# Performance work log

Measured on AMD Instinct MI355X. Metric: run time of the kernel, lower is better.

## Reference

```python
import jax, jax.numpy as jnp
import numpy as np

B, N, M, LDIM, RDIM, AGG = 4, 512, 512, 512, 512, 256


def setup_inputs() -> dict:
    key = jax.random.key(0)
    ks = jax.random.split(key, 7)
    data = jax.random.normal(ks[0], (B, N, LDIM), dtype=jnp.float32)
    crit = jax.random.normal(ks[1], (B, M, RDIM), dtype=jnp.float32)
    Wl = jax.random.normal(ks[2], (LDIM, AGG), dtype=jnp.float32) / np.sqrt(LDIM)
    bl = jax.random.normal(ks[3], (AGG,), dtype=jnp.float32) * 0.01
    Wr = jax.random.normal(ks[4], (RDIM, AGG), dtype=jnp.float32) / np.sqrt(RDIM)
    br = jax.random.normal(ks[5], (AGG,), dtype=jnp.float32) * 0.01
    agg = jax.random.uniform(ks[6], (AGG,), dtype=jnp.float32, minval=-0.01, maxval=0.01)
    return {"data": data, "crit": crit, "Wl": Wl, "bl": bl, "Wr": Wr, "br": br, "agg": agg}


def reference(data, crit, Wl, bl, Wr, br, agg):
    # linear projections
    datalin = jnp.einsum('bnl,la->bna', data, Wl) + bl   # [B,N,A]
    critlin = jnp.einsum('bmr,ra->bma', crit, Wr) + br   # [B,M,A]
    # broadcast add -> tanh -> reduce with agg vector: [B,N,M]
    linsum = jnp.tanh(datalin[:, :, None, :] + critlin[:, None, :, :])  # [B,N,M,A]
    dists = jnp.einsum('bnma,a->bnm', linsum, agg)
    return dists
```

## Files before the change

kernel.cpp:

```cpp
#include <hip/hip_runtime.h>


#define A_DIM 256
#define K_DIM 512
#define NROWS 2048

typedef unsigned short ushort;
typedef __attribute__((ext_vector_type(4))) unsigned short us4;
typedef __attribute__((ext_vector_type(8))) unsigned short us8;
typedef __attribute__((ext_vector_type(8))) short short8;
typedef __attribute__((ext_vector_type(4))) float f32x4;
typedef __attribute__((ext_vector_type(2))) float f32x2;

__device__ inline ushort f2bf(float x) {
    union { float f; unsigned u; } v; v.f = x;
    unsigned r = v.u + 0x7FFFu + ((v.u >> 16) & 1u);
    return (ushort)(r >> 16);
}
__device__ inline float bf2f(ushort h) {
    union { unsigned u; float f; } v; v.u = ((unsigned)h) << 16; return v.f;
}
__device__ inline unsigned pack2bf(float lo, float hi) {
    return (unsigned)f2bf(lo) | ((unsigned)f2bf(hi) << 16);
}
__device__ inline f32x2 fma2(f32x2 a, f32x2 b, f32x2 c) {
    return __builtin_elementwise_fma(a, b, c);
}

__global__ __launch_bounds__(256) void transpose_w_kernel(
    const float* __restrict__ Wl, const float* __restrict__ Wr,
    ushort* __restrict__ wt)
{
    __shared__ float tile[64][68];
    const int t   = threadIdx.x;
    const int bid = blockIdx.x;
    const int at  = bid & 3;
    const int kt  = (bid >> 2) & 7;
    const int src = bid >> 5;
    const int a0 = at * 64, k0 = kt * 64;
    const float* W = src ? Wr : Wl;
    ushort* out = wt + (size_t)src * (A_DIM * K_DIM);

    const int c4 = (t & 15) * 4;
    const int kr = t >> 4;
#pragma unroll
    for (int r = 0; r < 4; r++) {
        const int k = kr + r * 16;
        *(float4*)&tile[k][c4] = *(const float4*)(W + (size_t)(k0 + k) * A_DIM + a0 + c4);
    }
    __syncthreads();
    const int aL  = t & 63;
    const int ks0 = (t >> 6) * 16;
#pragma unroll
    for (int g = 0; g < 4; g++) {
        us4 o;
#pragma unroll
        for (int i = 0; i < 4; i++) o[i] = f2bf(tile[ks0 + g * 4 + i][aL]);
        __builtin_nontemporal_store(o, (us4*)(out + (size_t)(a0 + aL) * K_DIM + k0 + ks0 + g * 4));
    }
}

__global__ __launch_bounds__(256) void proj_mfma_kernel(
    const float* __restrict__ data, const float* __restrict__ crit,
    const float* __restrict__ bl, const float* __restrict__ br,
    const ushort* __restrict__ wt, ushort* __restrict__ eplanes)
{
    __shared__ ushort Ws[64][520];

    const int t   = threadIdx.x;
    const int bid = blockIdx.x;
    const int ct  = bid >> 7;
    const int rt  = bid & 127;
    const int src = rt >> 6;
    const int lr0 = (rt & 63) * 32;
    const int c0  = ct * 64;

    const float* X    = src ? crit : data;
    const float* bias = src ? br : bl;
    const ushort* Wt  = wt + (size_t)src * (A_DIM * K_DIM);
    ushort* E = eplanes + (size_t)src * ((size_t)A_DIM * NROWS);

    const int lane = t & 63;
    const int wid  = t >> 6;
    const int wm   = wid >> 1, wn = wid & 1;
    const int quad = lane >> 4, l16 = lane & 15;

    const float* xrow = X + (size_t)(lr0 + wm * 16 + l16) * K_DIM + quad * 8;
    const int aloc0 = wn * 32 + l16;

    f32x4 acc0 = {0.f, 0.f, 0.f, 0.f}, acc1 = {0.f, 0.f, 0.f, 0.f};

    {
        const int a  = t & 63;
        const int ks = (t >> 6) * 128;
        const ushort* s = Wt + (size_t)(c0 + a) * K_DIM + ks;
#pragma unroll
        for (int i = 0; i < 16; i++)
            *(us8*)&Ws[a][ks + i * 8] = *(const us8*)(s + i * 8);
    }

    float4 pa0 = *(const float4*)(xrow);
    float4 pb0 = *(const float4*)(xrow + 4);
    float4 pa1 = *(const float4*)(xrow + 32);
    float4 pb1 = *(const float4*)(xrow + 36);

    __syncthreads();

#pragma unroll
    for (int s = 0; s < 16; s++) {
        float4 ca = pa0, cb = pb0;
        pa0 = pa1; pb0 = pb1;
        if (s < 14) {
            pa1 = *(const float4*)(xrow + (s + 2) * 32);
            pb1 = *(const float4*)(xrow + (s + 2) * 32 + 4);
        }
        union { short8 s8; unsigned u[4]; } af;
        af.u[0] = pack2bf(ca.x, ca.y);
        af.u[1] = pack2bf(ca.z, ca.w);
        af.u[2] = pack2bf(cb.x, cb.y);
        af.u[3] = pack2bf(cb.z, cb.w);
        short8 b0 = *(const short8*)&Ws[aloc0     ][s * 32 + quad * 8];
        short8 b1 = *(const short8*)&Ws[aloc0 + 16][s * 32 + quad * 8];
        acc0 = __builtin_amdgcn_mfma_f32_16x16x32_bf16(af.s8, b0, acc0, 0, 0, 0);
        acc1 = __builtin_amdgcn_mfma_f32_16x16x32_bf16(af.s8, b1, acc1, 0, 0, 0);
    }

    const float c2 = 2.8853900817779268f;
    const int a_col0 = c0 + wn * 32 + l16;
    const int a_col1 = a_col0 + 16;
    const int row0   = lr0 + wm * 16 + quad * 4;
    const float bv0 = bias[a_col0], bv1 = bias[a_col1];
    us4 e0, e1;
#pragma unroll
    for (int i = 0; i < 4; i++) {
        float v0 = (acc0[i] + bv0) * c2;
        float v1 = (acc1[i] + bv1) * c2;
        v0 = fminf(fmaxf(v0, -15.f), 15.f);
        v1 = fminf(fmaxf(v1, -15.f), 15.f);
        e0[i] = f2bf(__builtin_amdgcn_exp2f(v0));
        e1[i] = f2bf(__builtin_amdgcn_exp2f(v1));
    }
    __builtin_nontemporal_store(e0, (us4*)(E + (size_t)a_col0 * NROWS + row0));
    __builtin_nontemporal_store(e1, (us4*)(E + (size_t)a_col1 * NROWS + row0));
}

__global__ __launch_bounds__(1024) void tanh_reduce_kernel(
    const ushort* __restrict__ eplanes, const float* __restrict__ agg,
    float* __restrict__ out)
{
    __shared__ __align__(16) float et [4][64][68];
    __shared__ __align__(16) float ect[4][64][68];
    __shared__ __align__(16) float aggs[256];

    const int t  = threadIdx.x;
    const int h  = t >> 8;
    const int u  = t & 255;
    const int m0 = blockIdx.x * 64;
    const int n0 = blockIdx.y * 64;
    const int b  = blockIdx.z;

    const size_t PLANE = (size_t)A_DIM * NROWS;
    const ushort* Ed = eplanes;
    const ushort* Ec = eplanes + PLANE;
    const int row_n = b * 512 + n0;
    const int row_m = b * 512 + m0;

    const int tx = u & 15;
    const int ty = u >> 4;

    if (t < 256) aggs[t] = 2.0f * agg[t];

    f32x2 acc2[4][2];
#pragma unroll
    for (int i = 0; i < 4; i++) { acc2[i][0] = (f32x2)0.f; acc2[i][1] = (f32x2)0.f; }
    float sagg = 0.f;

    const int aL = u >> 2;
    const int qd = u & 3;

    float (*eth)[68]  = et[h];
    float (*ecth)[68] = ect[h];

    {
        const size_t base = (size_t)(h * 64 + aL) * NROWS;
        us4 pn[4], pm[4];
#pragma unroll
        for (int r = 0; r < 4; r++) {
            pn[r] = *(const us4*)(Ed + base + row_n + qd * 16 + r * 4);
            pm[r] = *(const us4*)(Ec + base + row_m + qd * 16 + r * 4);
        }
#pragma unroll
        for (int r = 0; r < 4; r++) {
            float4 ev, cv;
            ev.x = bf2f(pn[r][0]); ev.y = bf2f(pn[r][1]);
            ev.z = bf2f(pn[r][2]); ev.w = bf2f(pn[r][3]);
            cv.x = bf2f(pm[r][0]); cv.y = bf2f(pm[r][1]);
            cv.z = bf2f(pm[r][2]); cv.w = bf2f(pm[r][3]);
            *(float4*)&eth [aL][qd * 16 + r * 4] = ev;
            *(float4*)&ecth[aL][qd * 16 + r * 4] = cv;
        }
    }
    __syncthreads();

    for (int qg = 0; qg < 16; qg++) {
        const float4 ag = *(const float4*)&aggs[h * 64 + qg * 4];
        sagg += (ag.x + ag.y) + (ag.z + ag.w);
        float  en[4][4];
        f32x2  fm[4][2];
#pragma unroll
        for (int v = 0; v < 4; v++) {
            float4 e4 = *(const float4*)&eth [qg * 4 + v][ty * 4];
            float4 f4 = *(const float4*)&ecth[qg * 4 + v][tx * 4];
            en[v][0] = e4.x; en[v][1] = e4.y; en[v][2] = e4.z; en[v][3] = e4.w;
            fm[v][0] = f32x2{f4.x, f4.y};
            fm[v][1] = f32x2{f4.z, f4.w};
        }
#pragma unroll
        for (int i = 0; i < 4; i++)
#pragma unroll
            for (int jp = 0; jp < 2; jp++) {
                const f32x2 one = (f32x2)1.f;
                f32x2 q0 = fma2((f32x2)en[0][i], fm[0][jp], one);
                f32x2 q1 = fma2((f32x2)en[1][i], fm[1][jp], one);
                f32x2 q2 = fma2((f32x2)en[2][i], fm[2][jp], one);
                f32x2 q3 = fma2((f32x2)en[3][i], fm[3][jp], one);
                f32x2 q01 = q0 * q1, q23 = q2 * q3;
                f32x2 n01 = fma2((f32x2)ag.x, q1, (f32x2)ag.y * q0);
                f32x2 n23 = fma2((f32x2)ag.z, q3, (f32x2)ag.w * q2);
                f32x2 N   = fma2(n01, q23, n23 * q01);
                f32x2 D   = q01 * q23;
                f32x2 r;
                r.x = __builtin_amdgcn_rcpf(D.x);
                r.y = __builtin_amdgcn_rcpf(D.y);
                acc2[i][jp] = fma2(N, r, acc2[i][jp]);
            }
    }

    const float base = 0.5f * sagg;
    float* xb = (float*)ect;
    __syncthreads();
    if (h != 0) {
        float* w = xb + ((size_t)(h - 1) * 256 + u) * 17;
#pragma unroll
        for (int i = 0; i < 4; i++)
#pragma unroll
            for (int jp = 0; jp < 2; jp++) {
                w[i * 4 + jp * 2 + 0] = base - acc2[i][jp].x;
                w[i * 4 + jp * 2 + 1] = base - acc2[i][jp].y;
            }
    }
    __syncthreads();
    if (h == 0) {
        const float* x1 = xb + (size_t)u * 17;
        const float* x2 = xb + ((size_t)256 + u) * 17;
        const float* x3 = xb + ((size_t)512 + u) * 17;
#pragma unroll
        for (int i = 0; i < 4; i++) {
            f32x4 v;
            v.x = ((base - acc2[i][0].x) + x1[i * 4 + 0]) + (x2[i * 4 + 0] + x3[i * 4 + 0]);
            v.y = ((base - acc2[i][0].y) + x1[i * 4 + 1]) + (x2[i * 4 + 1] + x3[i * 4 + 1]);
            v.z = ((base - acc2[i][1].x) + x1[i * 4 + 2]) + (x2[i * 4 + 2] + x3[i * 4 + 2]);
            v.w = ((base - acc2[i][1].y) + x1[i * 4 + 3]) + (x2[i * 4 + 3] + x3[i * 4 + 3]);
            __builtin_nontemporal_store(v,
                (f32x4*)(out + ((size_t)(b * 512 + n0 + ty * 4 + i) * 512) + m0 + tx * 4));
        }
    }
}

extern "C" void kernel_launch(void* const* d_in, const int* in_sizes, int n_in,
                              void* d_out, int out_size, void* d_ws, size_t ws_size,
                              hipStream_t stream) {
    const float* data = (const float*)d_in[0];
    const float* crit = (const float*)d_in[1];
    const float* Wl   = (const float*)d_in[2];
    const float* bl   = (const float*)d_in[3];
    const float* Wr   = (const float*)d_in[4];
    const float* br   = (const float*)d_in[5];
    const float* agg  = (const float*)d_in[6];
    float* out = (float*)d_out;

    ushort* eplanes = (ushort*)d_ws;
    ushort* wt      = eplanes + 2 * (size_t)A_DIM * NROWS;

    transpose_w_kernel<<<dim3(64), 256, 0, stream>>>(Wl, Wr, wt);

    proj_mfma_kernel<<<dim3(512), 256, 0, stream>>>(data, crit, bl, br, wt, eplanes);

    tanh_reduce_kernel<<<dim3(8, 8, 4), 1024, 0, stream>>>(eplanes, agg, out);
}
```

Before: 107.2 us.

## Fuse transpose, projection and tanh-reduce into one cooperative kernel

Merges the three kernels into a single cooperative launch of 256 blocks of 1024 threads, with grid.sync between the weight transpose, the MFMA projection and the tanh-reduce phases. Each phase is re-tiled so it fits 256 blocks: the transpose uses 16-wide tiles and the projection uses 64-row tiles with one MFMA accumulator per wave. Shared memory is shared between phases through a union. This removes two kernel launch gaps, at the cost of grid-wide barriers and smaller per-block work in the early phases.

```diff
diff --git a/kernel.cpp b/kernel.cpp
--- a/kernel.cpp
+++ b/kernel.cpp
@@ -1,4 +1,7 @@
 #include <hip/hip_runtime.h>
+#include <hip/hip_cooperative_groups.h>
+
+namespace cg = cooperative_groups;
 
 
 #define A_DIM 256
@@ -27,242 +30,223 @@
     return __builtin_elementwise_fma(a, b, c);
 }
 
-__global__ __launch_bounds__(256) void transpose_w_kernel(
-    const float* __restrict__ Wl, const float* __restrict__ Wr,
-    ushort* __restrict__ wt)
+__global__ __launch_bounds__(1024) void fused_fd_kernel(
+    const float* __restrict__ data, const float* __restrict__ crit,
+    const float* __restrict__ Wl, const float* __restrict__ bl,
+    const float* __restrict__ Wr, const float* __restrict__ br,
+    const float* __restrict__ agg,
+    ushort* __restrict__ wt, ushort* __restrict__ eplanes,
+    float* __restrict__ out)
 {
-    __shared__ float tile[64][68];
+    __shared__ __align__(16) union {
+        float tile[64][17];
+        ushort Ws[64][520];
+        struct { float et[4][64][68]; float ect[4][64][68];
+                 float aggs[256]; } p2;
+    } sm;
+
     const int t   = threadIdx.x;
     const int bid = blockIdx.x;
-    const int at  = bid & 3;
-    const int kt  = (bid >> 2) & 7;
-    const int src = bid >> 5;
-    const int a0 = at * 64, k0 = kt * 64;
-    const float* W = src ? Wr : Wl;
-    ushort* out = wt + (size_t)src * (A_DIM * K_DIM);
-
-    const int c4 = (t & 15) * 4;
-    const int kr = t >> 4;
-#pragma unroll
-    for (int r = 0; r < 4; r++) {
-        const int k = kr + r * 16;
-        *(float4*)&tile[k][c4] = *(const float4*)(W + (size_t)(k0 + k) * A_DIM + a0 + c4);
+    cg::grid_group grid = cg::this_grid();
+
+    {
+        const int at  = bid & 15;
+        const int kt  = (bid >> 4) & 7;
+        const int src = bid >> 7;
+        const int a0 = at * 16, k0 = kt * 64;
+        const float* W = src ? Wr : Wl;
+        ushort* o = wt + (size_t)src * (A_DIM * K_DIM);
+
+        const int k = t >> 4, ai = t & 15;
+        sm.tile[k][ai] = W[(size_t)(k0 + k) * A_DIM + a0 + ai];
+        __syncthreads();
+        const int a2 = t >> 6, kk = t & 63;
+        __builtin_nontemporal_store(f2bf(sm.tile[kk][a2]),
+                                    o + (size_t)(a0 + a2) * K_DIM + k0 + kk);
     }
-    __syncthreads();
-    const int aL  = t & 63;
-    const int ks0 = (t >> 6) * 16;
-#pragma unroll
-    for (int g = 0; g < 4; g++) {
-        us4 o;
-#pragma unroll
-        for (int i = 0; i < 4; i++) o[i] = f2bf(tile[ks0 + g * 4 + i][aL]);
-        __builtin_nontemporal_store(o, (us4*)(out + (size_t)(a0 + aL) * K_DIM + k0 + ks0 + g * 4));
+    grid.sync();
+
+    {
+        const int rt  = bid & 63;
+        const int ct  = bid >> 6;
+        const int src = rt >> 5;
+        const int lr0 = (rt & 31) * 64;
+        const int c0  = ct * 64;
+
+        const float* X    = src ? crit : data;
+        const float* bias = src ? br : bl;
+        const ushort* Wt  = wt + (size_t)src * (A_DIM * K_DIM);
+        ushort* E = eplanes + (size_t)src * ((size_t)A_DIM * NROWS);
+
+        const int lane = t & 63;
+        const int wid  = t >> 6;
+        const int wm   = wid >> 2, wn = wid & 3;
+        const int quad = lane >> 4, l16 = lane & 15;
+
+        const float* xrow = X + (size_t)(lr0 + wm * 16 + l16) * K_DIM + quad * 8;
+        const int aloc = wn * 16 + l16;
+
+        {
+            const int a  = t & 63;
+            const int ks = (t >> 6) * 32;
+            const ushort* s = Wt + (size_t)(c0 + a) * K_DIM + ks;
+#pragma unroll
+            for (int i = 0; i < 4; i++)
+                *(us8*)&sm.Ws[a][ks + i * 8] = *(const us8*)(s + i * 8);
+        }
+
+        f32x4 acc = {0.f, 0.f, 0.f, 0.f};
+        float4 pa0 = *(const float4*)(xrow);
+        float4 pb0 = *(const float4*)(xrow + 4);
+        float4 pa1 = *(const float4*)(xrow + 32);
+        float4 pb1 = *(const float4*)(xrow + 36);
+
+        __syncthreads();
+
+#pragma unroll
+        for (int s = 0; s < 16; s++) {
+            float4 ca = pa0, cb = pb0;
+            pa0 = pa1; pb0 = pb1;
+            if (s < 14) {
+                pa1 = *(const float4*)(xrow + (s + 2) * 32);
+                pb1 = *(const float4*)(xrow + (s + 2) * 32 + 4);
+            }
+            union { short8 s8; unsigned u[4]; } af;
+            af.u[0] = pack2bf(ca.x, ca.y);
+            af.u[1] = pack2bf(ca.z, ca.w);
+            af.u[2] = pack2bf(cb.x, cb.y);
+            af.u[3] = pack2bf(cb.z, cb.w);
+            short8 b0 = *(const short8*)&sm.Ws[aloc][s * 32 + quad * 8];
+            acc = __builtin_amdgcn_mfma_f32_16x16x32_bf16(af.s8, b0, acc, 0, 0, 0);
+        }
+
+        const float c2 = 2.8853900817779268f;
+        const int a_col = c0 + wn * 16 + l16;
+        const int row0  = lr0 + wm * 16 + quad * 4;
+        const float bv = bias[a_col];
+        us4 e0;
+#pragma unroll
+        for (int i = 0; i < 4; i++) {
+            float v0 = (acc[i] + bv) * c2;
+            v0 = fminf(fmaxf(v0, -15.f), 15.f);
+            e0[i] = f2bf(__builtin_amdgcn_exp2f(v0));
+        }
+        __builtin_nontemporal_store(e0, (us4*)(E + (size_t)a_col * NROWS + row0));
     }
-}
-
-__global__ __launch_bounds__(256) void proj_mfma_kernel(
-    const float* __restrict__ data, const float* __restrict__ crit,
-    const float* __restrict__ bl, const float* __restrict__ br,
-    const ushort* __restrict__ wt, ushort* __restrict__ eplanes)
-{
-    __shared__ ushort Ws[64][520];
-
-    const int t   = threadIdx.x;
-    const int bid = blockIdx.x;
-    const int ct  = bid >> 7;
-    const int rt  = bid & 127;
-    const int src = rt >> 6;
-    const int lr0 = (rt & 63) * 32;
-    const int c0  = ct * 64;
-
-    const float* X    = src ? crit : data;
-    const float* bias = src ? br : bl;
-    const ushort* Wt  = wt + (size_t)src * (A_DIM * K_DIM);
-    ushort* E = eplanes + (size_t)src * ((size_t)A_DIM * NROWS);
-
-    const int lane = t & 63;
-    const int wid  = t >> 6;
-    const int wm   = wid >> 1, wn = wid & 1;
-    const int quad = lane >> 4, l16 = lane & 15;
-
-    const float* xrow = X + (size_t)(lr0 + wm * 16 + l16) * K_DIM + quad * 8;
-    const int aloc0 = wn * 32 + l16;
-
-    f32x4 acc0 = {0.f, 0.f, 0.f, 0.f}, acc1 = {0.f, 0.f, 0.f, 0.f};
+    grid.sync();
 
     {
-        const int a  = t & 63;
-        const int ks = (t >> 6) * 128;
-        const ushort* s = Wt + (size_t)(c0 + a) * K_DIM + ks;
-#pragma unroll
-        for (int i = 0; i < 16; i++)
-            *(us8*)&Ws[a][ks + i * 8] = *(const us8*)(s + i * 8);
-    }
-
-    float4 pa0 = *(const float4*)(xrow);
-    float4 pb0 = *(const float4*)(xrow + 4);
-    float4 pa1 = *(const float4*)(xrow + 32);
-    float4 pb1 = *(const float4*)(xrow + 36);
-
-    __syncthreads();
-
-#pragma unroll
-    for (int s = 0; s < 16; s++) {
-        float4 ca = pa0, cb = pb0;
-        pa0 = pa1; pb0 = pb1;
-        if (s < 14) {
-            pa1 = *(const float4*)(xrow + (s + 2) * 32);
-            pb1 = *(const float4*)(xrow + (s + 2) * 32 + 4);
-        }
-        union { short8 s8; unsigned u[4]; } af;
-        af.u[0] = pack2bf(ca.x, ca.y);
-        af.u[1] = pack2bf(ca.z, ca.w);
-        af.u[2] = pack2bf(cb.x, cb.y);
-        af.u[3] = pack2bf(cb.z, cb.w);
-        short8 b0 = *(const short8*)&Ws[aloc0     ][s * 32 + quad * 8];
-        short8 b1 = *(const short8*)&Ws[aloc0 + 16][s * 32 + quad * 8];
-        acc0 = __builtin_amdgcn_mfma_f32_16x16x32_bf16(af.s8, b0, acc0, 0, 0, 0);
-        acc1 = __builtin_amdgcn_mfma_f32_16x16x32_bf16(af.s8, b1, acc1, 0, 0, 0);
-    }
-
-    const float c2 = 2.8853900817779268f;
-    const int a_col0 = c0 + wn * 32 + l16;
-    const int a_col1 = a_col0 + 16;
-    const int row0   = lr0 + wm * 16 + quad * 4;
-    const float bv0 = bias[a_col0], bv1 = bias[a_col1];
-    us4 e0, e1;
-#pragma unroll
-    for (int i = 0; i < 4; i++) {
-        float v0 = (acc0[i] + bv0) * c2;
-        float v1 = (acc1[i] + bv1) * c2;
-        v0 = fminf(fmaxf(v0, -15.f), 15.f);
-        v1 = fminf(fmaxf(v1, -15.f), 15.f);
-        e0[i] = f2bf(__builtin_amdgcn_exp2f(v0));
-        e1[i] = f2bf(__builtin_amdgcn_exp2f(v1));
-    }
-    __builtin_nontemporal_store(e0, (us4*)(E + (size_t)a_col0 * NROWS + row0));
-    __builtin_nontemporal_store(e1, (us4*)(E + (size_t)a_col1 * NROWS + row0));
-}
-
-__global__ __launch_bounds__(1024) void tanh_reduce_kernel(
-    const ushort* __restrict__ eplanes, const float* __restrict__ agg,
-    float* __restrict__ out)
-{
-    __shared__ __align__(16) float et [4][64][68];
-    __shared__ __align__(16) float ect[4][64][68];
-    __shared__ __align__(16) float aggs[256];
-
-    const int t  = threadIdx.x;
-    const int h  = t >> 8;
-    const int u  = t & 255;
-    const int m0 = blockIdx.x * 64;
-    const int n0 = blockIdx.y * 64;
-    const int b  = blockIdx.z;
-
-    const size_t PLANE = (size_t)A_DIM * NROWS;
-    const ushort* Ed = eplanes;
-    const ushort* Ec = eplanes + PLANE;
-    const int row_n = b * 512 + n0;
-    const int row_m = b * 512 + m0;
-
-    const int tx = u & 15;
-    const int ty = u >> 4;
-
-    if (t < 256) aggs[t] = 2.0f * agg[t];
-
-    f32x2 acc2[4][2];
-#pragma unroll
-    for (int i = 0; i < 4; i++) { acc2[i][0] = (f32x2)0.f; acc2[i][1] = (f32x2)0.f; }
-    float sagg = 0.f;
-
-    const int aL = u >> 2;
-    const int qd = u & 3;
-
-    float (*eth)[68]  = et[h];
-    float (*ecth)[68] = ect[h];
-
-    {
-        const size_t base = (size_t)(h * 64 + aL) * NROWS;
-        us4 pn[4], pm[4];
-#pragma unroll
-        for (int r = 0; r < 4; r++) {
-            pn[r] = *(const us4*)(Ed + base + row_n + qd * 16 + r * 4);
-            pm[r] = *(const us4*)(Ec + base + row_m + qd * 16 + r * 4);
-        }
-#pragma unroll
-        for (int r = 0; r < 4; r++) {
-            float4 ev, cv;
-            ev.x = bf2f(pn[r][0]); ev.y = bf2f(pn[r][1]);
-            ev.z = bf2f(pn[r][2]); ev.w = bf2f(pn[r][3]);
-            cv.x = bf2f(pm[r][0]); cv.y = bf2f(pm[r][1]);
-            cv.z = bf2f(pm[r][2]); cv.w = bf2f(pm[r][3]);
-            *(float4*)&eth [aL][qd * 16 + r * 4] = ev;
-            *(float4*)&ecth[aL][qd * 16 + r * 4] = cv;
-        }
-    }
-    __syncthreads();
-
-    for (int qg = 0; qg < 16; qg++) {
-        const float4 ag = *(const float4*)&aggs[h * 64 + qg * 4];
-        sagg += (ag.x + ag.y) + (ag.z + ag.w);
-        float  en[4][4];
-        f32x2  fm[4][2];
-#pragma unroll
-        for (int v = 0; v < 4; v++) {
-            float4 e4 = *(const float4*)&eth [qg * 4 + v][ty * 4];
-            float4 f4 = *(const float4*)&ecth[qg * 4 + v][tx * 4];
-            en[v][0] = e4.x; en[v][1] = e4.y; en[v][2] = e4.z; en[v][3] = e4.w;
-            fm[v][0] = f32x2{f4.x, f4.y};
-            fm[v][1] = f32x2{f4.z, f4.w};
-        }
-#pragma unroll
-        for (int i = 0; i < 4; i++)
-#pragma unroll
-            for (int jp = 0; jp < 2; jp++) {
-                const f32x2 one = (f32x2)1.f;
-                f32x2 q0 = fma2((f32x2)en[0][i], fm[0][jp], one);
-                f32x2 q1 = fma2((f32x2)en[1][i], fm[1][jp], one);
-                f32x2 q2 = fma2((f32x2)en[2][i], fm[2][jp], one);
-                f32x2 q3 = fma2((f32x2)en[3][i], fm[3][jp], one);
-                f32x2 q01 = q0 * q1, q23 = q2 * q3;
-                f32x2 n01 = fma2((f32x2)ag.x, q1, (f32x2)ag.y * q0);
-                f32x2 n23 = fma2((f32x2)ag.z, q3, (f32x2)ag.w * q2);
-                f32x2 N   = fma2(n01, q23, n23 * q01);
-                f32x2 D   = q01 * q23;
-                f32x2 r;
-                r.x = __builtin_amdgcn_rcpf(D.x);
-                r.y = __builtin_amdgcn_rcpf(D.y);
-                acc2[i][jp] = fma2(N, r, acc2[i][jp]);
-            }
-    }
-
-    const float base = 0.5f * sagg;
-    float* xb = (float*)ect;
-    __syncthreads();
-    if (h != 0) {
-        float* w = xb + ((size_t)(h - 1) * 256 + u) * 17;
-#pragma unroll
-        for (int i = 0; i < 4; i++)
-#pragma unroll
-            for (int jp = 0; jp < 2; jp++) {
-                w[i * 4 + jp * 2 + 0] = base - acc2[i][jp].x;
-                w[i * 4 + jp * 2 + 1] = base - acc2[i][jp].y;
-            }
-    }
-    __syncthreads();
-    if (h == 0) {
-        const float* x1 = xb + (size_t)u * 17;
-        const float* x2 = xb + ((size_t)256 + u) * 17;
-        const float* x3 = xb + ((size_t)512 + u) * 17;
-#pragma unroll
-        for (int i = 0; i < 4; i++) {
-            f32x4 v;
-            v.x = ((base - acc2[i][0].x) + x1[i * 4 + 0]) + (x2[i * 4 + 0] + x3[i * 4 + 0]);
-            v.y = ((base - acc2[i][0].y) + x1[i * 4 + 1]) + (x2[i * 4 + 1] + x3[i * 4 + 1]);
-            v.z = ((base - acc2[i][1].x) + x1[i * 4 + 2]) + (x2[i * 4 + 2] + x3[i * 4 + 2]);
-            v.w = ((base - acc2[i][1].y) + x1[i * 4 + 3]) + (x2[i * 4 + 3] + x3[i * 4 + 3]);
-            __builtin_nontemporal_store(v,
-                (f32x4*)(out + ((size_t)(b * 512 + n0 + ty * 4 + i) * 512) + m0 + tx * 4));
+        const int h  = t >> 8;
+        const int u  = t & 255;
+        const int m0 = (bid & 7) * 64;
+        const int n0 = ((bid >> 3) & 7) * 64;
+        const int b  = bid >> 6;
+
+        const size_t PLANE = (size_t)A_DIM * NROWS;
+        const ushort* Ed = eplanes;
+        const ushort* Ec = eplanes + PLANE;
+        const int row_n = b * 512 + n0;
+        const int row_m = b * 512 + m0;
+
+        const int tx = u & 15;
+        const int ty = u >> 4;
+
+        if (t < 256) sm.p2.aggs[t] = 2.0f * agg[t];
+
+        f32x2 acc2[4][2];
+#pragma unroll
+        for (int i = 0; i < 4; i++) { acc2[i][0] = (f32x2)0.f; acc2[i][1] = (f32x2)0.f; }
+        float sagg = 0.f;
+
+        const int aL = u >> 2;
+        const int qd = u & 3;
+
+        float (*eth)[68]  = sm.p2.et[h];
+        float (*ecth)[68] = sm.p2.ect[h];
+
+        {
+            const size_t base = (size_t)(h * 64 + aL) * NROWS;
+            us4 pn[4], pm[4];
+#pragma unroll
+            for (int r = 0; r < 4; r++) {
+                pn[r] = *(const us4*)(Ed + base + row_n + qd * 16 + r * 4);
+                pm[r] = *(const us4*)(Ec + base + row_m + qd * 16 + r * 4);
+            }
+#pragma unroll
+            for (int r = 0; r < 4; r++) {
+                float4 ev, cv;
+                ev.x = bf2f(pn[r][0]); ev.y = bf2f(pn[r][1]);
+                ev.z = bf2f(pn[r][2]); ev.w = bf2f(pn[r][3]);
+                cv.x = bf2f(pm[r][0]); cv.y = bf2f(pm[r][1]);
+                cv.z = bf2f(pm[r][2]); cv.w = bf2f(pm[r][3]);
+                *(float4*)&eth [aL][qd * 16 + r * 4] = ev;
+                *(float4*)&ecth[aL][qd * 16 + r * 4] = cv;
+            }
+        }
+        __syncthreads();
+
+        for (int qg = 0; qg < 16; qg++) {
+            const float4 ag = *(const float4*)&sm.p2.aggs[h * 64 + qg * 4];
+            sagg += (ag.x + ag.y) + (ag.z + ag.w);
+            float  en[4][4];
+            f32x2  fm[4][2];
+#pragma unroll
+            for (int v = 0; v < 4; v++) {
+                float4 e4 = *(const float4*)&eth [qg * 4 + v][ty * 4];
+                float4 f4 = *(const float4*)&ecth[qg * 4 + v][tx * 4];
+                en[v][0] = e4.x; en[v][1] = e4.y; en[v][2] = e4.z; en[v][3] = e4.w;
+                fm[v][0] = f32x2{f4.x, f4.y};
+                fm[v][1] = f32x2{f4.z, f4.w};
+            }
+#pragma unroll
+            for (int i = 0; i < 4; i++)
+#pragma unroll
+                for (int jp = 0; jp < 2; jp++) {
+                    const f32x2 one = (f32x2)1.f;
+                    f32x2 q0 = fma2((f32x2)en[0][i], fm[0][jp], one);
+                    f32x2 q1 = fma2((f32x2)en[1][i], fm[1][jp], one);
+                    f32x2 q2 = fma2((f32x2)en[2][i], fm[2][jp], one);
+                    f32x2 q3 = fma2((f32x2)en[3][i], fm[3][jp], one);
+                    f32x2 q01 = q0 * q1, q23 = q2 * q3;
+                    f32x2 n01 = fma2((f32x2)ag.x, q1, (f32x2)ag.y * q0);
+                    f32x2 n23 = fma2((f32x2)ag.z, q3, (f32x2)ag.w * q2);
+                    f32x2 N   = fma2(n01, q23, n23 * q01);
+                    f32x2 D   = q01 * q23;
+                    f32x2 r;
+                    r.x = __builtin_amdgcn_rcpf(D.x);
+                    r.y = __builtin_amdgcn_rcpf(D.y);
+                    acc2[i][jp] = fma2(N, r, acc2[i][jp]);
+                }
+        }
+
+        const float base = 0.5f * sagg;
+        float* xb = (float*)sm.p2.ect;
+        __syncthreads();
+        if (h != 0) {
+            float* w = xb + ((size_t)(h - 1) * 256 + u) * 17;
+#pragma unroll
+            for (int i = 0; i < 4; i++)
+#pragma unroll
+                for (int jp = 0; jp < 2; jp++) {
+                    w[i * 4 + jp * 2 + 0] = base - acc2[i][jp].x;
+                    w[i * 4 + jp * 2 + 1] = base - acc2[i][jp].y;
+                }
+        }
+        __syncthreads();
+        if (h == 0) {
+            const float* x1 = xb + (size_t)u * 17;
+            const float* x2 = xb + ((size_t)256 + u) * 17;
+            const float* x3 = xb + ((size_t)512 + u) * 17;
+#pragma unroll
+            for (int i = 0; i < 4; i++) {
+                f32x4 v;
+                v.x = ((base - acc2[i][0].x) + x1[i * 4 + 0]) + (x2[i * 4 + 0] + x3[i * 4 + 0]);
+                v.y = ((base - acc2[i][0].y) + x1[i * 4 + 1]) + (x2[i * 4 + 1] + x3[i * 4 + 1]);
+                v.z = ((base - acc2[i][1].x) + x1[i * 4 + 2]) + (x2[i * 4 + 2] + x3[i * 4 + 2]);
+                v.w = ((base - acc2[i][1].y) + x1[i * 4 + 3]) + (x2[i * 4 + 3] + x3[i * 4 + 3]);
+                __builtin_nontemporal_store(v,
+                    (f32x4*)(out + ((size_t)(b * 512 + n0 + ty * 4 + i) * 512) + m0 + tx * 4));
+            }
         }
     }
 }
@@ -282,9 +266,9 @@
     ushort* eplanes = (ushort*)d_ws;
     ushort* wt      = eplanes + 2 * (size_t)A_DIM * NROWS;
 
-    transpose_w_kernel<<<dim3(64), 256, 0, stream>>>(Wl, Wr, wt);
-
-    proj_mfma_kernel<<<dim3(512), 256, 0, stream>>>(data, crit, bl, br, wt, eplanes);
-
-    tanh_reduce_kernel<<<dim3(8, 8, 4), 1024, 0, stream>>>(eplanes, agg, out);
-}
+    void* args[] = { (void*)&data, (void*)&crit, (void*)&Wl, (void*)&bl,
+                     (void*)&Wr, (void*)&br, (void*)&agg,
+                     (void*)&wt, (void*)&eplanes, (void*)&out };
+    hipLaunchCooperativeKernel((void*)fused_fd_kernel, dim3(256), dim3(1024),
+                               args, 0, stream);
+}
```

New measurement: 181.4 us. 69.1% more time.

## Fuse weight transpose and bf16 conversion into projection kernel, halve LDS tile

Applied to the files above, without the earlier changes.

Removes the separate transpose kernel. Each projection block now loads fp32 weights directly, converts them to bf16 and transposes them into shared memory, working in two K-chunks of 256. This drops a kernel launch and the round-trip of the bf16 weight buffer through global memory. The smaller LDS tile plus launch_bounds(256,4) aims to raise occupancy. In exchange, all 512 blocks repeat the weight conversion and gain an extra barrier phase, and the fp32 weight reads double the bytes each block fetches.

```diff
diff --git a/kernel.cpp b/kernel.cpp
--- a/kernel.cpp
+++ b/kernel.cpp
@@ -27,45 +27,13 @@
     return __builtin_elementwise_fma(a, b, c);
 }
 
-__global__ __launch_bounds__(256) void transpose_w_kernel(
-    const float* __restrict__ Wl, const float* __restrict__ Wr,
-    ushort* __restrict__ wt)
+__global__ __launch_bounds__(256, 4) void proj_mfma_kernel(
+    const float* __restrict__ data, const float* __restrict__ crit,
+    const float* __restrict__ Wl, const float* __restrict__ bl,
+    const float* __restrict__ Wr, const float* __restrict__ br,
+    ushort* __restrict__ eplanes)
 {
-    __shared__ float tile[64][68];
-    const int t   = threadIdx.x;
-    const int bid = blockIdx.x;
-    const int at  = bid & 3;
-    const int kt  = (bid >> 2) & 7;
-    const int src = bid >> 5;
-    const int a0 = at * 64, k0 = kt * 64;
-    const float* W = src ? Wr : Wl;
-    ushort* out = wt + (size_t)src * (A_DIM * K_DIM);
-
-    const int c4 = (t & 15) * 4;
-    const int kr = t >> 4;
-#pragma unroll
-    for (int r = 0; r < 4; r++) {
-        const int k = kr + r * 16;
-        *(float4*)&tile[k][c4] = *(const float4*)(W + (size_t)(k0 + k) * A_DIM + a0 + c4);
-    }
-    __syncthreads();
-    const int aL  = t & 63;
-    const int ks0 = (t >> 6) * 16;
-#pragma unroll
-    for (int g = 0; g < 4; g++) {
-        us4 o;
-#pragma unroll
-        for (int i = 0; i < 4; i++) o[i] = f2bf(tile[ks0 + g * 4 + i][aL]);
-        __builtin_nontemporal_store(o, (us4*)(out + (size_t)(a0 + aL) * K_DIM + k0 + ks0 + g * 4));
-    }
-}
-
-__global__ __launch_bounds__(256) void proj_mfma_kernel(
-    const float* __restrict__ data, const float* __restrict__ crit,
-    const float* __restrict__ bl, const float* __restrict__ br,
-    const ushort* __restrict__ wt, ushort* __restrict__ eplanes)
-{
-    __shared__ ushort Ws[64][520];
+    __shared__ ushort Ws[64][264];
 
     const int t   = threadIdx.x;
     const int bid = blockIdx.x;
@@ -77,7 +45,7 @@
 
     const float* X    = src ? crit : data;
     const float* bias = src ? br : bl;
-    const ushort* Wt  = wt + (size_t)src * (A_DIM * K_DIM);
+    const float* W    = src ? Wr : Wl;
     ushort* E = eplanes + (size_t)src * ((size_t)A_DIM * NROWS);
 
     const int lane = t & 63;
@@ -88,41 +56,57 @@
     const float* xrow = X + (size_t)(lr0 + wm * 16 + l16) * K_DIM + quad * 8;
     const int aloc0 = wn * 32 + l16;
 
+    const int kq = lane >> 4;
+    const int aq = lane & 15;
+
     f32x4 acc0 = {0.f, 0.f, 0.f, 0.f}, acc1 = {0.f, 0.f, 0.f, 0.f};
-
-    {
-        const int a  = t & 63;
-        const int ks = (t >> 6) * 128;
-        const ushort* s = Wt + (size_t)(c0 + a) * K_DIM + ks;
-#pragma unroll
-        for (int i = 0; i < 16; i++)
-            *(us8*)&Ws[a][ks + i * 8] = *(const us8*)(s + i * 8);
-    }
 
     float4 pa0 = *(const float4*)(xrow);
     float4 pb0 = *(const float4*)(xrow + 4);
     float4 pa1 = *(const float4*)(xrow + 32);
     float4 pb1 = *(const float4*)(xrow + 36);
 
-    __syncthreads();
-
-#pragma unroll
-    for (int s = 0; s < 16; s++) {
-        float4 ca = pa0, cb = pb0;
-        pa0 = pa1; pb0 = pb1;
-        if (s < 14) {
-            pa1 = *(const float4*)(xrow + (s + 2) * 32);
-            pb1 = *(const float4*)(xrow + (s + 2) * 32 + 4);
-        }
-        union { short8 s8; unsigned u[4]; } af;
-        af.u[0] = pack2bf(ca.x, ca.y);
-        af.u[1] = pack2bf(ca.z, ca.w);
-        af.u[2] = pack2bf(cb.x, cb.y);
-        af.u[3] = pack2bf(cb.z, cb.w);
-        short8 b0 = *(const short8*)&Ws[aloc0     ][s * 32 + quad * 8];
-        short8 b1 = *(const short8*)&Ws[aloc0 + 16][s * 32 + quad * 8];
-        acc0 = __builtin_amdgcn_mfma_f32_16x16x32_bf16(af.s8, b0, acc0, 0, 0, 0);
-        acc1 = __builtin_amdgcn_mfma_f32_16x16x32_bf16(af.s8, b1, acc1, 0, 0, 0);
+    for (int kc = 0; kc < 2; kc++) {
+        __syncthreads();
+        {
+#pragma unroll
+            for (int p = 0; p < 4; p++) {
+                const int kb = wid * 64 + p * 16;
+                f32x4 v[4];
+#pragma unroll
+                for (int j = 0; j < 4; j++)
+                    v[j] = *(const f32x4*)(W + (size_t)(kc * 256 + kb + kq * 4 + j) * A_DIM
+                                             + c0 + aq * 4);
+#pragma unroll
+                for (int ai = 0; ai < 4; ai++) {
+                    us4 o;
+#pragma unroll
+                    for (int j = 0; j < 4; j++) o[j] = f2bf(v[j][ai]);
+                    *(us4*)&Ws[aq * 4 + ai][kb + kq * 4] = o;
+                }
+            }
+        }
+        __syncthreads();
+
+#pragma unroll
+        for (int ls = 0; ls < 8; ls++) {
+            const int s = kc * 8 + ls;
+            float4 ca = pa0, cb = pb0;
+            pa0 = pa1; pb0 = pb1;
+            if (s < 14) {
+                pa1 = *(const float4*)(xrow + (s + 2) * 32);
+                pb1 = *(const float4*)(xrow + (s + 2) * 32 + 4);
+            }
+            union { short8 s8; unsigned u[4]; } af;
+            af.u[0] = pack2bf(ca.x, ca.y);
+            af.u[1] = pack2bf(ca.z, ca.w);
+            af.u[2] = pack2bf(cb.x, cb.y);
+            af.u[3] = pack2bf(cb.z, cb.w);
+            short8 b0 = *(const short8*)&Ws[aloc0     ][ls * 32 + quad * 8];
+            short8 b1 = *(const short8*)&Ws[aloc0 + 16][ls * 32 + quad * 8];
+            acc0 = __builtin_amdgcn_mfma_f32_16x16x32_bf16(af.s8, b0, acc0, 0, 0, 0);
+            acc1 = __builtin_amdgcn_mfma_f32_16x16x32_bf16(af.s8, b1, acc1, 0, 0, 0);
+        }
     }
 
     const float c2 = 2.8853900817779268f;
@@ -280,11 +264,8 @@
     float* out = (float*)d_out;
 
     ushort* eplanes = (ushort*)d_ws;
-    ushort* wt      = eplanes + 2 * (size_t)A_DIM * NROWS;
-
-    transpose_w_kernel<<<dim3(64), 256, 0, stream>>>(Wl, Wr, wt);
-
-    proj_mfma_kernel<<<dim3(512), 256, 0, stream>>>(data, crit, bl, br, wt, eplanes);
+
+    proj_mfma_kernel<<<dim3(512), 256, 0, stream>>>(data, crit, Wl, bl, Wr, br, eplanes);
 
     tanh_reduce_kernel<<<dim3(8, 8, 4), 1024, 0, stream>>>(eplanes, agg, out);
 }
```

Result: no change. 105.8 us (-1.3%).
